# Optimization experiments

Hardware: AMD Instinct MI355X
Metric: run time of the kernel (lower is better)

## Reference

```python
import jax, jax.numpy as jnp
import numpy as np

B, S, E, H, D = 2, 2048, 1024, 16, 64  # batch, seq(=max_seq_len), embed_dim, heads, atten_dim


def setup_inputs() -> dict:
    key = jax.random.key(0)
    ks = jax.random.split(key, 9)
    s = 0.02
    return {
        "x": jax.random.normal(ks[0], (B, S, E), jnp.float32),
        "Wq": jax.random.normal(ks[1], (H, E, D), jnp.float32) * s,
        "Wk": jax.random.normal(ks[2], (H, E, D), jnp.float32) * s,
        "Wv": jax.random.normal(ks[3], (H, E, D), jnp.float32) * s,
        "bq": jax.random.normal(ks[4], (H, D), jnp.float32) * s,
        "bk": jax.random.normal(ks[5], (H, D), jnp.float32) * s,
        "bv": jax.random.normal(ks[6], (H, D), jnp.float32) * s,
        "Wp": jax.random.normal(ks[7], (H * D, E), jnp.float32) * s,
        "bp": jax.random.normal(ks[8], (E,), jnp.float32) * s,
    }


def reference(x, Wq, Wk, Wv, bq, bk, bv, Wp, bp):
    scale = jnp.sqrt(jnp.float32(D))
    # per-head projections, all heads at once: [B,H,S,D]
    q = jnp.einsum("bse,hed->bhsd", x, Wq) + bq[:, None, :]
    k = jnp.einsum("bse,hed->bhsd", x, Wk) + bk[:, None, :]
    v = jnp.einsum("bse,hed->bhsd", x, Wv) + bv[:, None, :]
    # causal scores [B,H,S,S], additive -inf mask above diagonal (as in the buffer)
    score = jnp.einsum("bhsd,bhtd->bhst", q, k) / scale
    mask = jnp.triu(jnp.full((S, S), -jnp.inf, jnp.float32), k=1)
    score = score + mask
    probs = jax.nn.softmax(score, axis=-1)
    attn = jnp.einsum("bhst,bhtd->bhsd", probs, v)
    # concat heads -> [B,S,H*D], then projection + ReLU
    concat = attn.transpose(0, 2, 1, 3).reshape(B, S, H * D)
    out = jax.nn.relu(concat @ Wp + bp)
    return out
```

## Files before the change

kernel.cpp:

```cpp
#include <hip/hip_runtime.h>

#define S_LEN 2048
#define E_DIM 1024
#define H_NUM 16
#define D_DIM 64

typedef unsigned short u16;
using bf16x8 = __attribute__((ext_vector_type(8))) short;
using f32x4  = __attribute__((ext_vector_type(4))) float;

#define MFMA16(A, B, C) __builtin_amdgcn_mfma_f32_16x16x32_bf16(A, B, C, 0, 0, 0)
#define QSCALE 0.18033688011112042f

__device__ __forceinline__ u16 f2bf(float f) {
    unsigned u = __float_as_uint(f);
    u += 0x7fffu + ((u >> 16) & 1u);
    return (u16)(u >> 16);
}
__device__ __forceinline__ f32x4 fzero4() { f32x4 z; z[0]=0.f; z[1]=0.f; z[2]=0.f; z[3]=0.f; return z; }

__device__ __forceinline__ unsigned cvtpk(float a, float b) {
    unsigned r;
    asm("v_cvt_pk_bf16_f32 %0, %1, %2" : "=v"(r) : "v"(a), "v"(b));
    return r;
}
__device__ __forceinline__ float fexp2(float x) {
#if __has_builtin(__builtin_amdgcn_exp2f)
    return __builtin_amdgcn_exp2f(x);
#else
    float r; asm("v_exp_f32 %0, %1" : "=v"(r) : "v"(x)); return r;
#endif
}
__device__ __forceinline__ float frcp(float x) {
#if __has_builtin(__builtin_amdgcn_rcpf)
    return __builtin_amdgcn_rcpf(x);
#else
    float r; asm("v_rcp_f32 %0, %1" : "=v"(r) : "v"(x)); return r;
#endif
}

__device__ __forceinline__ void gll16(const u16* g, u16* l) {
    __builtin_amdgcn_global_load_lds(
        (const __attribute__((address_space(1))) void*)g,
        (__attribute__((address_space(3))) void*)l, 16, 0, 0);
}

__device__ __forceinline__ void stage64(const u16* __restrict__ g, int gstride,
                                        u16* l, int wave, int lane) {
    #pragma unroll
    for (int i = 0; i < 2; i++) {
        const int r  = wave * 16 + i * 8 + (lane >> 3);
        const int sl = (lane & 7) ^ (r & 7);
        gll16(g + (size_t)r * gstride + sl * 8, l + (wave * 16 + i * 8) * 64);
    }
}
__device__ __forceinline__ bf16x8 ldswz(const u16* t, int rr, int hh, int quad) {
    const int sl = ((hh << 2) + quad) ^ (rr & 7);
    return *(const bf16x8*)(t + rr * 64 + sl * 8);
}

__global__ __launch_bounds__(256) void cvt_bf16(const float* __restrict__ in, u16* __restrict__ outp, int n) {
    int i4 = (blockIdx.x * 256 + threadIdx.x) * 4;
    if (i4 < n) {
        float4 f = *(const float4*)(in + i4);
        unsigned lo = (unsigned)f2bf(f.x) | ((unsigned)f2bf(f.y) << 16);
        unsigned hi = (unsigned)f2bf(f.z) | ((unsigned)f2bf(f.w) << 16);
        uint2 p; p.x = lo; p.y = hi;
        *(uint2*)(outp + i4) = p;
    }
}

__device__ __forceinline__ void cvt_t_tile(const float* __restrict__ bin, u16* __restrict__ bout,
                                           int R, int C, int r0, int c0) {
    __shared__ float t[64][65];
    const int tid = threadIdx.x;
    const int lr = tid >> 2, lc = (tid & 3) * 16;

    const float* src = bin + (size_t)(r0 + lr) * C + c0 + lc;
    #pragma unroll
    for (int j = 0; j < 4; j++) {
        float4 f = *(const float4*)(src + j * 4);
        t[lr][lc + j * 4 + 0] = f.x; t[lr][lc + j * 4 + 1] = f.y;
        t[lr][lc + j * 4 + 2] = f.z; t[lr][lc + j * 4 + 3] = f.w;
    }
    __syncthreads();

    u16* dst = bout + (size_t)(c0 + lr) * R + r0 + lc;
    u16 vals[16];
    #pragma unroll
    for (int i = 0; i < 16; i++) vals[i] = f2bf(t[lc + i][lr]);
    uint4 pa, pb;
    pa.x = vals[0] | (vals[1] << 16);  pa.y = vals[2] | (vals[3] << 16);
    pa.z = vals[4] | (vals[5] << 16);  pa.w = vals[6] | (vals[7] << 16);
    pb.x = vals[8] | (vals[9] << 16);  pb.y = vals[10] | (vals[11] << 16);
    pb.z = vals[12] | (vals[13] << 16); pb.w = vals[14] | (vals[15] << 16);
    *(uint4*)dst = pa;
    *(uint4*)(dst + 8) = pb;
}

__global__ __launch_bounds__(256) void cvt_bf16_t(const float* __restrict__ in, u16* __restrict__ outp,
                                                  int R, int C) {
    const float* bin = in + (size_t)blockIdx.z * R * C;
    u16* bout = outp + (size_t)blockIdx.z * R * C;
    cvt_t_tile(bin, bout, R, C, blockIdx.y * 64, blockIdx.x * 64);
}

__global__ __launch_bounds__(256) void cvt_w3_t(
    const float* __restrict__ Wq, const float* __restrict__ Wk, const float* __restrict__ Wv,
    u16* __restrict__ wqt, u16* __restrict__ wkt, u16* __restrict__ wvt) {
    const int which = blockIdx.z >> 4, bh = blockIdx.z & 15;
    const float* in = (which == 0) ? Wq : (which == 1) ? Wk : Wv;
    u16* outp = (which == 0) ? wqt : (which == 1) ? wkt : wvt;
    const float* bin = in + (size_t)bh * E_DIM * D_DIM;
    u16* bout = outp + (size_t)bh * E_DIM * D_DIM;
    cvt_t_tile(bin, bout, E_DIM, D_DIM, blockIdx.y * 64, 0);
}

__global__ __launch_bounds__(256) void qkv_gemm(
    const u16* __restrict__ xb, const u16* __restrict__ wcat,
    const float* __restrict__ bq, const float* __restrict__ bk, const float* __restrict__ bv,
    u16* __restrict__ oq, u16* __restrict__ okk, u16* __restrict__ ov)
{
    const int m0 = blockIdx.x * 128;
    const int n0 = blockIdx.y * 128;

    __shared__ u16 As[128 * 32];
    __shared__ u16 Bs[128 * 32];

    const int tid  = threadIdx.x;
    const int wave = tid >> 6, lane = tid & 63, quad = lane >> 4, l16 = lane & 15;
    const int mh = wave >> 1, nh = wave & 1;

    const int lrow = lane >> 2, lcol = (lane & 3) * 8;
    const u16* aBase = xb   + (size_t)(m0 + wave * 32 + lrow) * E_DIM + lcol;
    const u16* bBase = wcat + (size_t)(n0 + wave * 32 + lrow) * E_DIM + lcol;
    u16* aLds0 = &As[(wave * 32     ) * 32];
    u16* aLds1 = &As[(wave * 32 + 16) * 32];
    u16* bLds0 = &Bs[(wave * 32     ) * 32];
    u16* bLds1 = &Bs[(wave * 32 + 16) * 32];

    f32x4 acc[4][4];
    #pragma unroll
    for (int j = 0; j < 4; j++)
        #pragma unroll
        for (int mi = 0; mi < 4; mi++) acc[j][mi] = fzero4();

    for (int k0 = 0; k0 < E_DIM; k0 += 32) {
        __syncthreads();
        gll16(aBase + k0,                 aLds0);
        gll16(aBase + k0 + 16 * E_DIM,    aLds1);
        gll16(bBase + k0,                 bLds0);
        gll16(bBase + k0 + 16 * E_DIM,    bLds1);
        __syncthreads();

        bf16x8 af[4];
        #pragma unroll
        for (int mi = 0; mi < 4; mi++)
            af[mi] = *(const bf16x8*)(&As[(mh * 64 + mi * 16 + l16) * 32 + quad * 8]);
        #pragma unroll
        for (int j = 0; j < 4; j++) {
            bf16x8 bfv = *(const bf16x8*)(&Bs[(nh * 64 + j * 16 + l16) * 32 + quad * 8]);
            #pragma unroll
            for (int mi = 0; mi < 4; mi++)
                acc[j][mi] = MFMA16(af[mi], bfv, acc[j][mi]);
        }
    }

    const int t = n0 >> 10;
    if (t < 2) {
        const float scl = (t == 0) ? QSCALE : 1.0f;
        const float* bias = (t == 0) ? bq : bk;
        u16* dst = (t == 0) ? oq : okk;
        #pragma unroll
        for (int j = 0; j < 4; j++) {
            const int n = n0 + nh * 64 + j * 16 + l16;
            const int h = (n >> 6) & 15, d = n & 63;
            float bia = bias[h * D_DIM + d];
            #pragma unroll
            for (int mi = 0; mi < 4; mi++) {
                #pragma unroll
                for (int r = 0; r < 4; r++) {
                    int m = m0 + mh * 64 + mi * 16 + quad * 4 + r;
                    int b = m >> 11, s = m & 2047;
                    dst[((size_t)(b * H_NUM + h) * S_LEN + s) * D_DIM + d] =
                        f2bf((acc[j][mi][r] + bia) * scl);
                }
            }
        }
    } else {
        #pragma unroll
        for (int j = 0; j < 4; j++) {
            const int n = n0 + nh * 64 + j * 16 + l16;
            const int h = (n >> 6) & 15, d = n & 63;
            float bia = bv[h * D_DIM + d];
            #pragma unroll
            for (int mi = 0; mi < 4; mi++) {
                int m = m0 + mh * 64 + mi * 16 + quad * 4;
                int b = m >> 11, s = m & 2047;
                uint2 pk;
                pk.x = cvtpk(acc[j][mi][0] + bia, acc[j][mi][1] + bia);
                pk.y = cvtpk(acc[j][mi][2] + bia, acc[j][mi][3] + bia);
                *(uint2*)(&ov[((size_t)(b * H_NUM + h) * D_DIM + d) * S_LEN + s]) = pk;
            }
        }
    }
}

__global__ __launch_bounds__(256) void attn_fwd(
    const u16* __restrict__ q, const u16* __restrict__ k, const u16* __restrict__ vt,
    u16* __restrict__ concat)
{
    const int p  = blockIdx.x;
    const int qa = p, qb = 31 - p;
    const int h  = blockIdx.y;
    const int bb = blockIdx.z;

    const size_t headoff = (size_t)(bb * H_NUM + h) * S_LEN * D_DIM;
    const u16* qh  = q  + headoff;
    const u16* kh  = k  + headoff;
    const u16* vth = vt + headoff;

    __shared__ u16 QaL[64 * 64];
    __shared__ u16 QbL[64 * 64];
    __shared__ u16 Ks[2][64 * 64];
    __shared__ u16 Vts[2][64 * 64];
    __shared__ u16 Ps[4][16 * 72];

    const int tid  = threadIdx.x;
    const int wave = tid >> 6, lane = tid & 63, quad = lane >> 4, l16 = lane & 15;

    stage64(qh + (size_t)qa * 64 * D_DIM, D_DIM, QaL,    wave, lane);
    stage64(qh + (size_t)qb * 64 * D_DIM, D_DIM, QbL,    wave, lane);
    stage64(kh,                           D_DIM, Ks[0],  wave, lane);
    stage64(vth,                          S_LEN, Vts[0], wave, lane);
    __syncthreads();

    bf16x8 bqa0 = ldswz(QaL, wave * 16 + l16, 0, quad);
    bf16x8 bqa1 = ldswz(QaL, wave * 16 + l16, 1, quad);
    bf16x8 bqb0 = ldswz(QbL, wave * 16 + l16, 0, quad);
    bf16x8 bqb1 = ldswz(QbL, wave * 16 + l16, 1, quad);

    f32x4 oa[4], ob[4];
    #pragma unroll
    for (int nt = 0; nt < 4; nt++) { oa[nt] = fzero4(); ob[nt] = fzero4(); }
    float la = 0.f, lb = 0.f;

    const int qga = qa * 64 + wave * 16 + l16;
    const int qgb = qb * 64 + wave * 16 + l16;

    for (int kt = 0; kt <= qb; kt++) {
        if (kt) __syncthreads();
        if (kt < qb) {
            stage64(kh + (size_t)(kt + 1) * 64 * D_DIM, D_DIM, Ks[(kt + 1) & 1],  wave, lane);
            stage64(vth + (kt + 1) * 64,                S_LEN, Vts[(kt + 1) & 1], wave, lane);
        }
        const u16* Kc = Ks[kt & 1];
        const u16* Vc = Vts[kt & 1];
        const bool both = (kt <= qa);

        f32x4 stb[4], sta[4];
        #pragma unroll
        for (int nt = 0; nt < 4; nt++) {
            const int rr = nt * 16 + l16;
            bf16x8 ak0 = ldswz(Kc, rr, 0, quad);
            bf16x8 ak1 = ldswz(Kc, rr, 1, quad);
            stb[nt] = MFMA16(ak0, bqb0, fzero4());
            stb[nt] = MFMA16(ak1, bqb1, stb[nt]);
            if (both) {
                sta[nt] = MFMA16(ak0, bqa0, fzero4());
                sta[nt] = MFMA16(ak1, bqa1, sta[nt]);
            }
        }

        bf16x8 bv0[4], bv1[4];

        {
            u16* pw = &Ps[wave][0];
            #pragma unroll
            for (int nt = 0; nt < 4; nt++) {
                float pe[4];
                if (kt == qb) {
                    #pragma unroll
                    for (int r = 0; r < 4; r++) {
                        int kkg = kt * 64 + nt * 16 + quad * 4 + r;
                        pe[r] = (kkg > qgb) ? 0.f : fexp2(stb[nt][r]);
                    }
                } else {
                    #pragma unroll
                    for (int r = 0; r < 4; r++) pe[r] = fexp2(stb[nt][r]);
                }
                lb += (pe[0] + pe[1]) + (pe[2] + pe[3]);
                uint2 pk;
                pk.x = cvtpk(pe[0], pe[1]);
                pk.y = cvtpk(pe[2], pe[3]);
                *(uint2*)(&pw[l16 * 72 + nt * 16 + quad * 4]) = pk;
            }
            bf16x8 ap0 = *(const bf16x8*)(&Ps[wave][l16 * 72 + quad * 8]);
            bf16x8 ap1 = *(const bf16x8*)(&Ps[wave][l16 * 72 + 32 + quad * 8]);
            #pragma unroll
            for (int nt = 0; nt < 4; nt++) {
                bv0[nt] = ldswz(Vc, nt * 16 + l16, 0, quad);
                bv1[nt] = ldswz(Vc, nt * 16 + l16, 1, quad);
                ob[nt] = MFMA16(ap0, bv0[nt], ob[nt]);
                ob[nt] = MFMA16(ap1, bv1[nt], ob[nt]);
            }
        }

        if (both) {
            u16* pw = &Ps[wave][0];
            #pragma unroll
            for (int nt = 0; nt < 4; nt++) {
                float pe[4];
                if (kt == qa) {
                    #pragma unroll
                    for (int r = 0; r < 4; r++) {
                        int kkg = kt * 64 + nt * 16 + quad * 4 + r;
                        pe[r] = (kkg > qga) ? 0.f : fexp2(sta[nt][r]);
                    }
                } else {
                    #pragma unroll
                    for (int r = 0; r < 4; r++) pe[r] = fexp2(sta[nt][r]);
                }
                la += (pe[0] + pe[1]) + (pe[2] + pe[3]);
                uint2 pk;
                pk.x = cvtpk(pe[0], pe[1]);
                pk.y = cvtpk(pe[2], pe[3]);
                *(uint2*)(&pw[l16 * 72 + nt * 16 + quad * 4]) = pk;
            }
            bf16x8 ap0 = *(const bf16x8*)(&Ps[wave][l16 * 72 + quad * 8]);
            bf16x8 ap1 = *(const bf16x8*)(&Ps[wave][l16 * 72 + 32 + quad * 8]);
            #pragma unroll
            for (int nt = 0; nt < 4; nt++) {
                oa[nt] = MFMA16(ap0, bv0[nt], oa[nt]);
                oa[nt] = MFMA16(ap1, bv1[nt], oa[nt]);
            }
        }
    }

    lb += __shfl_xor(lb, 16); lb += __shfl_xor(lb, 32);
    la += __shfl_xor(la, 16); la += __shfl_xor(la, 32);

    #pragma unroll
    for (int r = 0; r < 4; r++) {
        const int srcl = quad * 4 + r;
        float lbi = frcp(__shfl(lb, srcl));
        float lai = frcp(__shfl(la, srcl));
        int sqa = qa * 64 + wave * 16 + quad * 4 + r;
        int sqb = qb * 64 + wave * 16 + quad * 4 + r;
        #pragma unroll
        for (int nt = 0; nt < 4; nt++) {
            concat[((size_t)(bb * S_LEN + sqa)) * E_DIM + h * D_DIM + nt * 16 + l16] =
                f2bf(oa[nt][r] * lai);
            concat[((size_t)(bb * S_LEN + sqb)) * E_DIM + h * D_DIM + nt * 16 + l16] =
                f2bf(ob[nt][r] * lbi);
        }
    }
}

__global__ __launch_bounds__(256) void out_proj(
    const u16* __restrict__ concat, const u16* __restrict__ wpt,
    const float* __restrict__ bp, float* __restrict__ out)
{
    const int m0 = blockIdx.x * 128;
    const int n0 = blockIdx.y * 128;

    __shared__ u16 As[128 * 40];
    __shared__ u16 Bs[128 * 40];

    const int tid  = threadIdx.x;
    const int wave = tid >> 6, lane = tid & 63, quad = lane >> 4, l16 = lane & 15;
    const int mh = wave >> 1, nh = wave & 1;

    const int arow = tid >> 1, acol = (tid & 1) * 16;

    const u16* aptr = concat + (size_t)(m0 + arow) * E_DIM + acol;
    const u16* bptr = wpt + (size_t)(n0 + arow) * E_DIM + acol;

    f32x4 acc[4][4];
    #pragma unroll
    for (int j = 0; j < 4; j++)
        #pragma unroll
        for (int mi = 0; mi < 4; mi++) acc[j][mi] = fzero4();

    uint4 pA0, pA1, pB0, pB1;
    pA0 = *(const uint4*)(aptr);     pA1 = *(const uint4*)(aptr + 8);
    pB0 = *(const uint4*)(bptr);     pB1 = *(const uint4*)(bptr + 8);

    for (int k0 = 0; k0 < E_DIM; k0 += 32) {
        __syncthreads();
        *(uint4*)(&As[arow * 40 + acol    ]) = pA0;
        *(uint4*)(&As[arow * 40 + acol + 8]) = pA1;
        *(uint4*)(&Bs[arow * 40 + acol    ]) = pB0;
        *(uint4*)(&Bs[arow * 40 + acol + 8]) = pB1;
        __syncthreads();

        if (k0 + 32 < E_DIM) {
            pA0 = *(const uint4*)(aptr + k0 + 32);  pA1 = *(const uint4*)(aptr + k0 + 40);
            pB0 = *(const uint4*)(bptr + k0 + 32);  pB1 = *(const uint4*)(bptr + k0 + 40);
        }

        bf16x8 af[4];
        #pragma unroll
        for (int mi = 0; mi < 4; mi++)
            af[mi] = *(const bf16x8*)(&As[(mh * 64 + mi * 16 + l16) * 40 + quad * 8]);
        #pragma unroll
        for (int j = 0; j < 4; j++) {
            bf16x8 bfv = *(const bf16x8*)(&Bs[(nh * 64 + j * 16 + l16) * 40 + quad * 8]);
            #pragma unroll
            for (int mi = 0; mi < 4; mi++)
                acc[j][mi] = MFMA16(af[mi], bfv, acc[j][mi]);
        }
    }

    #pragma unroll
    for (int j = 0; j < 4; j++) {
        int n = n0 + nh * 64 + j * 16 + l16;
        float bia = bp[n];
        #pragma unroll
        for (int mi = 0; mi < 4; mi++) {
            #pragma unroll
            for (int r = 0; r < 4; r++) {
                int m = m0 + mh * 64 + mi * 16 + quad * 4 + r;
                out[(size_t)m * E_DIM + n] = fmaxf(acc[j][mi][r] + bia, 0.f);
            }
        }
    }
}

extern "C" void kernel_launch(void* const* d_in, const int* in_sizes, int n_in,
                              void* d_out, int out_size, void* d_ws, size_t ws_size,
                              hipStream_t stream)
{
    (void)in_sizes; (void)n_in; (void)out_size; (void)ws_size;
    const float* x  = (const float*)d_in[0];
    const float* Wq = (const float*)d_in[1];
    const float* Wk = (const float*)d_in[2];
    const float* Wv = (const float*)d_in[3];
    const float* bq = (const float*)d_in[4];
    const float* bk = (const float*)d_in[5];
    const float* bv = (const float*)d_in[6];
    const float* Wp = (const float*)d_in[7];
    const float* bp = (const float*)d_in[8];
    float* out = (float*)d_out;

    const size_t QKV_ELEMS = (size_t)2 * H_NUM * S_LEN * D_DIM;
    const size_t W_ELEMS   = (size_t)H_NUM * E_DIM * D_DIM;

    u16* q   = (u16*)d_ws;
    u16* k   = q   + QKV_ELEMS;
    u16* v   = k   + QKV_ELEMS;
    u16* cc  = v   + QKV_ELEMS;
    u16* xb  = cc  + QKV_ELEMS;
    u16* wqt = xb  + QKV_ELEMS;
    u16* wkt = wqt + W_ELEMS;
    u16* wvt = wkt + W_ELEMS;
    u16* wpt = wvt + W_ELEMS;

    cvt_bf16<<<dim3(4096), 256, 0, stream>>>(x, xb, (int)QKV_ELEMS);
    cvt_w3_t<<<dim3(1, 16, 48), 256, 0, stream>>>(Wq, Wk, Wv, wqt, wkt, wvt);
    cvt_bf16_t<<<dim3(16, 16, 1), 256, 0, stream>>>(Wp, wpt, H_NUM * D_DIM, E_DIM);

    qkv_gemm<<<dim3(32, 24), 256, 0, stream>>>(xb, wqt, bq, bk, bv, q, k, v);
    attn_fwd<<<dim3(16, 16, 2), 256, 0, stream>>>(q, k, v, cc);
    out_proj<<<dim3(32, 8), 256, 0, stream>>>(cc, wpt, bp, out);
}
```

Baseline: 207.1 us.

## Process four query tiles per attention block and coalesce V-transpose stores via LDS

```diff
diff --git a/kernel.cpp b/kernel.cpp
--- a/kernel.cpp
+++ b/kernel.cpp
@@ -124,8 +124,8 @@
     const int m0 = blockIdx.x * 128;
     const int n0 = blockIdx.y * 128;
 
-    __shared__ u16 As[128 * 32];
-    __shared__ u16 Bs[128 * 32];
+    __shared__ u16 As[128 * 36];
+    __shared__ u16 Bs[128 * 36];
 
     const int tid  = threadIdx.x;
     const int wave = tid >> 6, lane = tid & 63, quad = lane >> 4, l16 = lane & 15;
@@ -188,171 +188,176 @@
             }
         }
     } else {
-        #pragma unroll
-        for (int j = 0; j < 4; j++) {
-            const int n = n0 + nh * 64 + j * 16 + l16;
-            const int h = (n >> 6) & 15, d = n & 63;
-            float bia = bv[h * D_DIM + d];
-            #pragma unroll
-            for (int mi = 0; mi < 4; mi++) {
-                int m = m0 + mh * 64 + mi * 16 + quad * 4;
-                int b = m >> 11, s = m & 2047;
-                uint2 pk;
-                pk.x = cvtpk(acc[j][mi][0] + bia, acc[j][mi][1] + bia);
-                pk.y = cvtpk(acc[j][mi][2] + bia, acc[j][mi][3] + bia);
-                *(uint2*)(&ov[((size_t)(b * H_NUM + h) * D_DIM + d) * S_LEN + s]) = pk;
-            }
-        }
-    }
-}
-
-__global__ __launch_bounds__(256) void attn_fwd(
+        const int b  = m0 >> 11, s0 = m0 & 2047;
+        const int h0 = (n0 >> 6) & 15;
+        u16* Tb0 = As;
+        u16* Tb1 = Bs;
+        #pragma unroll
+        for (int pass = 0; pass < 2; ++pass) {
+            __syncthreads();
+            if (mh == pass) {
+                u16* Tb = nh ? Tb1 : Tb0;
+                #pragma unroll
+                for (int j = 0; j < 4; j++) {
+                    const int n = n0 + nh * 64 + j * 16 + l16;
+                    const int d = n & 63, hh = (n >> 6) & 15;
+                    const float bia = bv[hh * D_DIM + d];
+                    const int nl = j * 16 + l16;
+                    #pragma unroll
+                    for (int mi = 0; mi < 4; mi++) {
+                        uint2 pk;
+                        pk.x = cvtpk(acc[j][mi][0] + bia, acc[j][mi][1] + bia);
+                        pk.y = cvtpk(acc[j][mi][2] + bia, acc[j][mi][3] + bia);
+                        *(uint2*)(&Tb[nl * 72 + mi * 16 + quad * 4]) = pk;
+                    }
+                }
+            }
+            __syncthreads();
+            #pragma unroll
+            for (int g = 0; g < 4; ++g) {
+                const int rowi = g * 32 + (tid >> 3);
+                const int ml = (tid & 7) * 8;
+                const u16* srcp = (rowi < 64 ? Tb0 : Tb1) + (rowi & 63) * 72 + ml;
+                const int hh = h0 + (rowi >> 6), d = rowi & 63;
+                u16* dstp = ov + ((size_t)(b * H_NUM + hh) * D_DIM + d) * S_LEN
+                               + s0 + pass * 64 + ml;
+                *(uint4*)dstp = *(const uint4*)srcp;
+            }
+        }
+    }
+}
+
+__global__ __launch_bounds__(256, 1) void attn_fwd(
     const u16* __restrict__ q, const u16* __restrict__ k, const u16* __restrict__ vt,
     u16* __restrict__ concat)
 {
-    const int p  = blockIdx.x;
-    const int qa = p, qb = 31 - p;
-    const int h  = blockIdx.y;
-    const int bb = blockIdx.z;
+    const int bid = blockIdx.x;
+    const int p   = (bid >> 3) & 7;
+    const int g   = (bid & 7) * 4 + (bid >> 6);
+    const int h   = g & 15;
+    const int bb  = g >> 4;
+
+    const int qtv[4] = { p, 15 - p, 16 + p, 31 - p };
 
     const size_t headoff = (size_t)(bb * H_NUM + h) * S_LEN * D_DIM;
     const u16* qh  = q  + headoff;
     const u16* kh  = k  + headoff;
     const u16* vth = vt + headoff;
 
-    __shared__ u16 QaL[64 * 64];
-    __shared__ u16 QbL[64 * 64];
+    __shared__ u16 QL[4][64 * 64];
     __shared__ u16 Ks[2][64 * 64];
     __shared__ u16 Vts[2][64 * 64];
-    __shared__ u16 Ps[4][16 * 72];
 
     const int tid  = threadIdx.x;
     const int wave = tid >> 6, lane = tid & 63, quad = lane >> 4, l16 = lane & 15;
 
-    stage64(qh + (size_t)qa * 64 * D_DIM, D_DIM, QaL,    wave, lane);
-    stage64(qh + (size_t)qb * 64 * D_DIM, D_DIM, QbL,    wave, lane);
-    stage64(kh,                           D_DIM, Ks[0],  wave, lane);
-    stage64(vth,                          S_LEN, Vts[0], wave, lane);
+    #pragma unroll
+    for (int t = 0; t < 4; ++t)
+        stage64(qh + (size_t)qtv[t] * 64 * D_DIM, D_DIM, QL[t], wave, lane);
+    stage64(kh,  D_DIM, Ks[0],  wave, lane);
+    stage64(vth, S_LEN, Vts[0], wave, lane);
     __syncthreads();
 
-    bf16x8 bqa0 = ldswz(QaL, wave * 16 + l16, 0, quad);
-    bf16x8 bqa1 = ldswz(QaL, wave * 16 + l16, 1, quad);
-    bf16x8 bqb0 = ldswz(QbL, wave * 16 + l16, 0, quad);
-    bf16x8 bqb1 = ldswz(QbL, wave * 16 + l16, 1, quad);
-
-    f32x4 oa[4], ob[4];
-    #pragma unroll
-    for (int nt = 0; nt < 4; nt++) { oa[nt] = fzero4(); ob[nt] = fzero4(); }
-    float la = 0.f, lb = 0.f;
-
-    const int qga = qa * 64 + wave * 16 + l16;
-    const int qgb = qb * 64 + wave * 16 + l16;
-
-    for (int kt = 0; kt <= qb; kt++) {
-        if (kt) __syncthreads();
-        if (kt < qb) {
+    bf16x8 bq0[4], bq1[4];
+    #pragma unroll
+    for (int t = 0; t < 4; ++t) {
+        bq0[t] = ldswz(QL[t], wave * 16 + l16, 0, quad);
+        bq1[t] = ldswz(QL[t], wave * 16 + l16, 1, quad);
+    }
+
+    u16* Psw = &QL[0][0] + wave * 1152;
+
+    f32x4 o[4][4];
+    #pragma unroll
+    for (int t = 0; t < 4; ++t)
+        #pragma unroll
+        for (int nt = 0; nt < 4; ++nt) o[t][nt] = fzero4();
+    float ls[4] = {0.f, 0.f, 0.f, 0.f};
+
+    const int qrow = wave * 16 + l16;
+
+    for (int kt = 0; kt <= qtv[3]; ++kt) {
+        __syncthreads();
+        if (kt < qtv[3]) {
             stage64(kh + (size_t)(kt + 1) * 64 * D_DIM, D_DIM, Ks[(kt + 1) & 1],  wave, lane);
             stage64(vth + (kt + 1) * 64,                S_LEN, Vts[(kt + 1) & 1], wave, lane);
         }
         const u16* Kc = Ks[kt & 1];
         const u16* Vc = Vts[kt & 1];
-        const bool both = (kt <= qa);
-
-        f32x4 stb[4], sta[4];
-        #pragma unroll
-        for (int nt = 0; nt < 4; nt++) {
+        const bool act[4] = { kt <= qtv[0], kt <= qtv[1], kt <= qtv[2], true };
+
+        f32x4 st[4][4];
+        #pragma unroll
+        for (int nt = 0; nt < 4; ++nt) {
             const int rr = nt * 16 + l16;
             bf16x8 ak0 = ldswz(Kc, rr, 0, quad);
             bf16x8 ak1 = ldswz(Kc, rr, 1, quad);
-            stb[nt] = MFMA16(ak0, bqb0, fzero4());
-            stb[nt] = MFMA16(ak1, bqb1, stb[nt]);
-            if (both) {
-                sta[nt] = MFMA16(ak0, bqa0, fzero4());
-                sta[nt] = MFMA16(ak1, bqa1, sta[nt]);
+            #pragma unroll
+            for (int t = 3; t >= 0; --t) {
+                if (act[t]) {
+                    st[t][nt] = MFMA16(ak0, bq0[t], fzero4());
+                    st[t][nt] = MFMA16(ak1, bq1[t], st[t][nt]);
+                }
             }
         }
 
         bf16x8 bv0[4], bv1[4];
-
-        {
-            u16* pw = &Ps[wave][0];
-            #pragma unroll
-            for (int nt = 0; nt < 4; nt++) {
-                float pe[4];
-                if (kt == qb) {
-                    #pragma unroll
-                    for (int r = 0; r < 4; r++) {
-                        int kkg = kt * 64 + nt * 16 + quad * 4 + r;
-                        pe[r] = (kkg > qgb) ? 0.f : fexp2(stb[nt][r]);
+        #pragma unroll
+        for (int nt = 0; nt < 4; ++nt) {
+            bv0[nt] = ldswz(Vc, nt * 16 + l16, 0, quad);
+            bv1[nt] = ldswz(Vc, nt * 16 + l16, 1, quad);
+        }
+
+        #pragma unroll
+        for (int t = 3; t >= 0; --t) {
+            if (act[t]) {
+                const int qti = qtv[t];
+                #pragma unroll
+                for (int nt = 0; nt < 4; ++nt) {
+                    float pe[4];
+                    if (kt == qti) {
+                        #pragma unroll
+                        for (int r = 0; r < 4; ++r) {
+                            int kkg = kt * 64 + nt * 16 + quad * 4 + r;
+                            pe[r] = (kkg > qti * 64 + qrow) ? 0.f : fexp2(st[t][nt][r]);
+                        }
+                    } else {
+                        #pragma unroll
+                        for (int r = 0; r < 4; ++r) pe[r] = fexp2(st[t][nt][r]);
                     }
-                } else {
-                    #pragma unroll
-                    for (int r = 0; r < 4; r++) pe[r] = fexp2(stb[nt][r]);
+                    ls[t] += (pe[0] + pe[1]) + (pe[2] + pe[3]);
+                    uint2 pk;
+                    pk.x = cvtpk(pe[0], pe[1]);
+                    pk.y = cvtpk(pe[2], pe[3]);
+                    *(uint2*)(&Psw[l16 * 72 + nt * 16 + quad * 4]) = pk;
                 }
-                lb += (pe[0] + pe[1]) + (pe[2] + pe[3]);
-                uint2 pk;
-                pk.x = cvtpk(pe[0], pe[1]);
-                pk.y = cvtpk(pe[2], pe[3]);
-                *(uint2*)(&pw[l16 * 72 + nt * 16 + quad * 4]) = pk;
-            }
-            bf16x8 ap0 = *(const bf16x8*)(&Ps[wave][l16 * 72 + quad * 8]);
-            bf16x8 ap1 = *(const bf16x8*)(&Ps[wave][l16 * 72 + 32 + quad * 8]);
-            #pragma unroll
-            for (int nt = 0; nt < 4; nt++) {
-                bv0[nt] = ldswz(Vc, nt * 16 + l16, 0, quad);
-                bv1[nt] = ldswz(Vc, nt * 16 + l16, 1, quad);
-                ob[nt] = MFMA16(ap0, bv0[nt], ob[nt]);
-                ob[nt] = MFMA16(ap1, bv1[nt], ob[nt]);
-            }
-        }
-
-        if (both) {
-            u16* pw = &Ps[wave][0];
-            #pragma unroll
-            for (int nt = 0; nt < 4; nt++) {
-                float pe[4];
-                if (kt == qa) {
-                    #pragma unroll
-                    for (int r = 0; r < 4; r++) {
-                        int kkg = kt * 64 + nt * 16 + quad * 4 + r;
-                        pe[r] = (kkg > qga) ? 0.f : fexp2(sta[nt][r]);
-                    }
-                } else {
-                    #pragma unroll
-                    for (int r = 0; r < 4; r++) pe[r] = fexp2(sta[nt][r]);
+                bf16x8 ap0 = *(const bf16x8*)(&Psw[l16 * 72 + quad * 8]);
+                bf16x8 ap1 = *(const bf16x8*)(&Psw[l16 * 72 + 32 + quad * 8]);
+                #pragma unroll
+                for (int nt = 0; nt < 4; ++nt) {
+                    o[t][nt] = MFMA16(ap0, bv0[nt], o[t][nt]);
+                    o[t][nt] = MFMA16(ap1, bv1[nt], o[t][nt]);
                 }
-                la += (pe[0] + pe[1]) + (pe[2] + pe[3]);
-                uint2 pk;
-                pk.x = cvtpk(pe[0], pe[1]);
-                pk.y = cvtpk(pe[2], pe[3]);
-                *(uint2*)(&pw[l16 * 72 + nt * 16 + quad * 4]) = pk;
-            }
-            bf16x8 ap0 = *(const bf16x8*)(&Ps[wave][l16 * 72 + quad * 8]);
-            bf16x8 ap1 = *(const bf16x8*)(&Ps[wave][l16 * 72 + 32 + quad * 8]);
-            #pragma unroll
-            for (int nt = 0; nt < 4; nt++) {
-                oa[nt] = MFMA16(ap0, bv0[nt], oa[nt]);
-                oa[nt] = MFMA16(ap1, bv1[nt], oa[nt]);
-            }
-        }
-    }
-
-    lb += __shfl_xor(lb, 16); lb += __shfl_xor(lb, 32);
-    la += __shfl_xor(la, 16); la += __shfl_xor(la, 32);
-
-    #pragma unroll
-    for (int r = 0; r < 4; r++) {
-        const int srcl = quad * 4 + r;
-        float lbi = frcp(__shfl(lb, srcl));
-        float lai = frcp(__shfl(la, srcl));
-        int sqa = qa * 64 + wave * 16 + quad * 4 + r;
-        int sqb = qb * 64 + wave * 16 + quad * 4 + r;
-        #pragma unroll
-        for (int nt = 0; nt < 4; nt++) {
-            concat[((size_t)(bb * S_LEN + sqa)) * E_DIM + h * D_DIM + nt * 16 + l16] =
-                f2bf(oa[nt][r] * lai);
-            concat[((size_t)(bb * S_LEN + sqb)) * E_DIM + h * D_DIM + nt * 16 + l16] =
-                f2bf(ob[nt][r] * lbi);
+            }
+        }
+    }
+
+    #pragma unroll
+    for (int t = 0; t < 4; ++t) {
+        ls[t] += __shfl_xor(ls[t], 16);
+        ls[t] += __shfl_xor(ls[t], 32);
+    }
+    #pragma unroll
+    for (int t = 0; t < 4; ++t) {
+        const int sq0 = qtv[t] * 64 + wave * 16;
+        #pragma unroll
+        for (int r = 0; r < 4; ++r) {
+            float li = frcp(__shfl(ls[t], quad * 4 + r));
+            int sq = sq0 + quad * 4 + r;
+            #pragma unroll
+            for (int nt = 0; nt < 4; ++nt)
+                concat[((size_t)(bb * S_LEN + sq)) * E_DIM + h * D_DIM + nt * 16 + l16] =
+                    f2bf(o[t][nt][r] * li);
         }
     }
 }
@@ -461,6 +466,6 @@
     cvt_bf16_t<<<dim3(16, 16, 1), 256, 0, stream>>>(Wp, wpt, H_NUM * D_DIM, E_DIM);
 
     qkv_gemm<<<dim3(32, 24), 256, 0, stream>>>(xb, wqt, bq, bk, bv, q, k, v);
-    attn_fwd<<<dim3(16, 16, 2), 256, 0, stream>>>(q, k, v, cc);
+    attn_fwd<<<dim3(256), 256, 0, stream>>>(q, k, v, cc);
     out_proj<<<dim3(32, 8), 256, 0, stream>>>(cc, wpt, bp, out);
 }
```

After: 220.4 us. 1.06x slower.
